# Optimization experiments

Hardware: AMD Instinct MI355X
Metric: run time of the kernel (lower is better)

The kernel has to match this reference:

```python
import jax, jax.numpy as jnp
import numpy as np

# Module hyperparameters (from init_kwargs)
KH = KW = 3
STRIDE = 2
PAD = 1
OUT_PAD = 1
DIL = 1
IN_LEN = 8   # length of each input capsule
OUT_LEN = 8  # length of each output capsule
N_IN_CAPS = 64 // IN_LEN    # 8
N_OUT_CAPS = 64 // OUT_LEN  # 8
NUM_ITERATIONS = 3


def _squash(x):
    # v * |v|^2 / ((1 + |v|^2) * |v|), along last (capsule-length) dim
    sn = jnp.sum(x * x, axis=-1, keepdims=True)
    return x * (sn / ((1.0 + sn) * jnp.sqrt(sn + 1e-12)))


def _k_means_routing(priors, num_iterations):
    # priors: [..., K, M] ; soft k-means routing with 'dot' similarity,
    # softmax over the votes dim K (softmax_dim=-2), squash at the end.
    out = jnp.mean(priors, axis=-2, keepdims=True)          # [..., 1, M]
    for _ in range(num_iterations):
        nrm = jnp.linalg.norm(out, axis=-1, keepdims=True)
        out_n = out / jnp.maximum(nrm, 1e-12)               # F.normalize(p=2)
        logits = jnp.sum(priors * out_n, axis=-1, keepdims=True)  # [..., K, 1]
        probs = jax.nn.softmax(logits, axis=-2)
        out = jnp.sum(probs * priors, axis=-2, keepdims=True)
    return _squash(out)[..., 0, :]                          # [..., M]


def setup_inputs() -> dict:
    key = jax.random.key(0)
    k1, k2, k3 = jax.random.split(key, 3)
    input = jax.random.normal(k1, (2, 64, 32, 32), dtype=jnp.float32)
    # weight: (in_length, out_channels//out_length, out_length, kh, kw)
    weight = jax.random.normal(k2, (IN_LEN, N_OUT_CAPS, OUT_LEN, KH, KW), dtype=jnp.float32) * 0.1
    # bias: (out_channels//out_length, out_length)
    bias = jax.random.normal(k3, (N_OUT_CAPS, OUT_LEN), dtype=jnp.float32) * 0.1
    return {"input": input, "weight": weight, "bias": bias}


def reference(input, weight, bias):
    n, c_in, h_in, w_in = input.shape
    fi = c_in // IN_LEN
    fo = weight.shape[1]
    # conv_transpose == conv(lhs-dilated input, spatially flipped kernel)
    pad_lo = DIL * (KH - 1) - PAD
    patches = jax.lax.conv_general_dilated_patches(
        input, (KH, KW), (1, 1),
        padding=((pad_lo, pad_lo + OUT_PAD), (pad_lo, pad_lo + OUT_PAD)),
        lhs_dilation=(STRIDE, STRIDE), rhs_dilation=(DIL, DIL))
    ho, wo = patches.shape[-2], patches.shape[-1]
    # feature dim of patches is ordered (c, kh, kw), channel-major
    patches = patches.reshape(n, fi, IN_LEN, KH, KW, ho, wo)
    w_flip = weight[..., ::-1, ::-1]  # [IN_LEN, fo, OUT_LEN, KH, KW]
    # votes: each (input capsule, kernel tap) casts a vote per output capsule
    priors = jnp.einsum('nflhwpq,lgmhw->npqgfhwm', patches, w_flip)
    priors = priors.reshape(n, ho, wo, fo, fi * KH * KW, OUT_LEN)
    out = _k_means_routing(priors, NUM_ITERATIONS)  # [n, ho, wo, fo, OUT_LEN]
    out = out + bias                                # bias: [fo, OUT_LEN]
    out = out.reshape(n, ho, wo, fo * OUT_LEN).transpose(0, 3, 1, 2)
    return out  # [n, out_channels, ho, wo] = [2, 64, 64, 64]
```

## Files before the change

kernel.cpp:

```cpp
#include <hip/hip_runtime.h>
#include <math.h>

#define HIN 32
#define WIN 32
#define NITER 3

__global__ __launch_bounds__(256) void transpose_in(const float* __restrict__ in,
                                                    float* __restrict__ tin) {
    __shared__ float lds[64 * 33];
    const int t = threadIdx.x;
    const int n = blockIdx.x >> 5;
    const int s0 = (blockIdx.x & 31) << 5;
    const float* ib = in + n * 65536;
    float* ob = tin + n * 65536;
#pragma unroll
    for (int k = 0; k < 8; ++k) {
        int idx = k * 256 + t;
        int c = idx >> 5, sl = idx & 31;
        lds[c * 33 + sl] = ib[c * 1024 + s0 + sl];
    }
    __syncthreads();
#pragma unroll
    for (int k = 0; k < 8; ++k) {
        int idx = k * 256 + t;
        int sl = idx >> 6, c = idx & 63;
        ob[(size_t)(s0 + sl) * 64 + c] = lds[c * 33 + sl];
    }
}

template <int CTRL>
__device__ __forceinline__ float dpp_add(float v) {
    int p = __builtin_amdgcn_update_dpp(0, __float_as_int(v), CTRL, 0xF, 0xF, true);
    return v + __int_as_float(p);
}
__device__ __forceinline__ float sum8(float v) {
    v = dpp_add<0xB1>(v);
    v = dpp_add<0x4E>(v);
    v = dpp_add<0x141>(v);
    return v;
}

template <int TH, int TW>
__device__ __forceinline__ void route_path(
    const float* __restrict__ tin, const float* __restrict__ wlds,
    const float* __restrict__ bias, float* __restrict__ olds,
    int n, int p, int q, int g, int s, int lane, int wave) {
    constexpr int T = TH * TW;
    constexpr float Z = (float)(72 - 8 * T);

    float pri[T][8];
#pragma unroll
    for (int i = 0; i < TH; ++i) {
        const int h = (TH == 1) ? 1 : i * 2;
        const int y = (p + h - 1) >> 1;
#pragma unroll
        for (int j = 0; j < TW; ++j) {
            const int w = (TW == 1) ? 1 : j * 2;
            const int x = (q + w - 1) >> 1;
            const int v = i * TW + j;
            const bool valid = (y < HIN) && (x < WIN);
            if (valid) {
                float xv[8];
                const float4* xp =
                    (const float4*)(tin + (((size_t)n * HIN + y) * WIN + x) * 64 + s * 8);
                float4 x0 = xp[0], x1 = xp[1];
                xv[0] = x0.x; xv[1] = x0.y; xv[2] = x0.z; xv[3] = x0.w;
                xv[4] = x1.x; xv[5] = x1.y; xv[6] = x1.z; xv[7] = x1.w;
                const int tap = h * 3 + w;
                const float* wb = wlds + (tap * 8 + g) * 64;
#pragma unroll
                for (int m = 0; m < 8; ++m) {
                    const float4* wp = (const float4*)(wb + ((m + g) & 7) * 8);
                    float4 w0 = wp[0], w1 = wp[1];
                    pri[v][m] = xv[0] * w0.x + xv[1] * w0.y + xv[2] * w0.z + xv[3] * w0.w +
                                xv[4] * w1.x + xv[5] * w1.y + xv[6] * w1.z + xv[7] * w1.w;
                }
            } else {
#pragma unroll
                for (int m = 0; m < 8; ++m) pri[v][m] = 0.f;
            }
        }
    }

    float o[8];
#pragma unroll
    for (int m = 0; m < 8; ++m) {
        float a = 0.f;
#pragma unroll
        for (int v = 0; v < T; ++v) a += pri[v][m];
        o[m] = sum8(a) * (1.f / 72.f);
    }

#pragma unroll
    for (int it = 0; it < NITER; ++it) {
        float sn = 0.f;
#pragma unroll
        for (int m = 0; m < 8; ++m) sn += o[m] * o[m];
        const float inv = __builtin_amdgcn_rsqf(fmaxf(sn, 1e-24f));
        float on[8];
#pragma unroll
        for (int m = 0; m < 8; ++m) on[m] = o[m] * inv;

        float r[9];
        r[8] = 0.f;
        float e[T];
#pragma unroll
        for (int v = 0; v < T; ++v) {
            float a = 0.f;
#pragma unroll
            for (int m = 0; m < 8; ++m) a += pri[v][m] * on[m];
            e[v] = __expf(a);
            r[8] += e[v];
        }
#pragma unroll
        for (int m = 0; m < 8; ++m) {
            float a = 0.f;
#pragma unroll
            for (int v = 0; v < T; ++v) a += e[v] * pri[v][m];
            r[m] = a;
        }
#pragma unroll
        for (int j = 0; j < 9; ++j) r[j] = sum8(r[j]);
        const float invs = __builtin_amdgcn_rcpf(r[8] + Z);
#pragma unroll
        for (int m = 0; m < 8; ++m) o[m] = r[m] * invs;
    }

    float sn = 0.f;
#pragma unroll
    for (int m = 0; m < 8; ++m) sn += o[m] * o[m];
    const float factor =
        sn * __builtin_amdgcn_rcpf(1.f + sn) * __builtin_amdgcn_rsqf(sn + 1e-12f);

    float val = o[0];
#pragma unroll
    for (int m = 1; m < 8; ++m)
        if (s == m) val = o[m];
    val = val * factor + bias[g * 8 + s];

    olds[lane * 5 + wave] = val;
}

__global__ __launch_bounds__(256) void caps_routing(
    const float* __restrict__ tin, const float* __restrict__ weight,
    const float* __restrict__ bias, float* __restrict__ out) {
    __shared__ float wlds[4608];
    __shared__ float olds[64 * 5];
    const int t = threadIdx.x;

    {
        const int l = t & 7;
        const int g8 = (t >> 3) & 7;
        const int c = t >> 6;
        const float* wsrc = weight + ((l * 8 + g8) * 8 + c * 2) * 9;
        float* wd = wlds + g8 * 64 + l;
#pragma unroll
        for (int mi = 0; mi < 2; ++mi) {
            const int mg = ((c * 2 + mi + g8) & 7) * 8;
#pragma unroll
            for (int kh = 0; kh < 3; ++kh)
#pragma unroll
                for (int kw = 0; kw < 3; ++kw) {
                    const int tap = (2 - kh) * 3 + (2 - kw);
                    wd[tap * 512 + mg] = wsrc[mi * 9 + kh * 3 + kw];
                }
        }
    }
    __syncthreads();

    const int wave = t >> 6;
    const int lane = t & 63;
    const int g = lane >> 3;
    const int s = lane & 7;

    const int b = blockIdx.x;
    const int n = b >> 10;
    const int p = (b >> 4) & 63;
    const int j = b & 15;
    const int qpar = j >> 3;
    const int qb = (j & 7) * 8 + qpar;
    const int q = qb + 2 * wave;

    if (p & 1) {
        if (qpar)
            route_path<2, 2>(tin, wlds, bias, olds, n, p, q, g, s, lane, wave);
        else
            route_path<2, 1>(tin, wlds, bias, olds, n, p, q, g, s, lane, wave);
    } else {
        if (qpar)
            route_path<1, 2>(tin, wlds, bias, olds, n, p, q, g, s, lane, wave);
        else
            route_path<1, 1>(tin, wlds, bias, olds, n, p, q, g, s, lane, wave);
    }

    __syncthreads();
    const int c2 = t >> 2, w = t & 3;
    out[(((size_t)n * 64 + c2) * 64 + p) * 64 + qb + 2 * w] = olds[c2 * 5 + w];
}

extern "C" void kernel_launch(void* const* d_in, const int* in_sizes, int n_in,
                              void* d_out, int out_size, void* d_ws, size_t ws_size,
                              hipStream_t stream) {
    const float* in = (const float*)d_in[0];
    const float* weight = (const float*)d_in[1];
    const float* bias = (const float*)d_in[2];
    float* out = (float*)d_out;
    float* tin = (float*)d_ws;

    transpose_in<<<64, 256, 0, stream>>>(in, tin);
    caps_routing<<<2048, 256, 0, stream>>>(tin, weight, bias, out);
}
```

Baseline: 75.49 us.

## Pre-permute weights in prep kernel and load only needed taps per block

Weight flipping and permutation move out of every routing block into one extra block of the prep kernel, which writes a pre-laid-out weight buffer to workspace. Each routing block then copies only the T taps its parity class needs (up to 4 of 9) into a smaller LDS array with contiguous float4 copies, replacing the strided scalar scatter of all 9 taps. The routing loop is also reorganized so the normalization by the softmax sum is applied only once at the end, because the direction-only normalize makes the per-iteration scale redundant. This cuts per-block prologue global loads, LDS writes and LDS footprint, at the cost of an extra workspace buffer and a dependency on the prep kernel.

```diff
diff --git a/kernel.cpp b/kernel.cpp
--- a/kernel.cpp
+++ b/kernel.cpp
@@ -4,27 +4,48 @@
 #define HIN 32
 #define WIN 32
 #define NITER 3
-
-__global__ __launch_bounds__(256) void transpose_in(const float* __restrict__ in,
-                                                    float* __restrict__ tin) {
+#define TIN_ELEMS 131072
+
+__global__ __launch_bounds__(256) void prep(const float* __restrict__ in,
+                                            const float* __restrict__ weight,
+                                            float* __restrict__ tin,
+                                            float* __restrict__ wprep) {
     __shared__ float lds[64 * 33];
+    const int b = blockIdx.x;
     const int t = threadIdx.x;
-    const int n = blockIdx.x >> 5;
-    const int s0 = (blockIdx.x & 31) << 5;
-    const float* ib = in + n * 65536;
-    float* ob = tin + n * 65536;
-#pragma unroll
-    for (int k = 0; k < 8; ++k) {
-        int idx = k * 256 + t;
-        int c = idx >> 5, sl = idx & 31;
-        lds[c * 33 + sl] = ib[c * 1024 + s0 + sl];
-    }
-    __syncthreads();
-#pragma unroll
-    for (int k = 0; k < 8; ++k) {
-        int idx = k * 256 + t;
-        int sl = idx >> 6, c = idx & 63;
-        ob[(size_t)(s0 + sl) * 64 + c] = lds[c * 33 + sl];
+    if (b < 64) {
+        const int n = b >> 5;
+        const int s0 = (b & 31) << 5;
+        const float* ib = in + n * 65536;
+        float* ob = tin + n * 65536;
+#pragma unroll
+        for (int k = 0; k < 8; ++k) {
+            int idx = k * 256 + t;
+            int c = idx >> 5, sl = idx & 31;
+            lds[c * 33 + sl] = ib[c * 1024 + s0 + sl];
+        }
+        __syncthreads();
+#pragma unroll
+        for (int k = 0; k < 8; ++k) {
+            int idx = k * 256 + t;
+            int sl = idx >> 6, c = idx & 63;
+            ob[(size_t)(s0 + sl) * 64 + c] = lds[c * 33 + sl];
+        }
+    } else {
+#pragma unroll
+        for (int k = 0; k < 2; ++k) {
+            const int lgm = k * 256 + t;
+            const int l = lgm >> 6, g = (lgm >> 3) & 7, m = lgm & 7;
+            const float* src = weight + lgm * 9;
+            float* drow = wprep + g * 64 + ((m + g) & 7) * 8 + l;
+#pragma unroll
+            for (int kh = 0; kh < 3; ++kh)
+#pragma unroll
+                for (int kw = 0; kw < 3; ++kw) {
+                    const int tap = (2 - kh) * 3 + (2 - kw);
+                    drow[tap * 512] = src[kh * 3 + kw];
+                }
+        }
     }
 }
 
@@ -41,12 +62,31 @@
 }
 
 template <int TH, int TW>
-__device__ __forceinline__ void route_path(
-    const float* __restrict__ tin, const float* __restrict__ wlds,
-    const float* __restrict__ bias, float* __restrict__ olds,
-    int n, int p, int q, int g, int s, int lane, int wave) {
+__device__ __forceinline__ void run_path(
+    const float* __restrict__ tin, const float* __restrict__ wprep,
+    const float* __restrict__ bias, float* __restrict__ out,
+    float* __restrict__ wlds, float* __restrict__ olds,
+    int t, int n, int p, int qb) {
     constexpr int T = TH * TW;
     constexpr float Z = (float)(72 - 8 * T);
+
+    const int wave = t >> 6;
+    const int lane = t & 63;
+
+    if (wave < T) {
+        const int hh = (TH == 1) ? 1 : ((TW == 2 ? (wave >> 1) : wave) * 2);
+        const int ww = (TW == 1) ? 1 : ((wave & 1) * 2);
+        const float4* src = (const float4*)(wprep + (hh * 3 + ww) * 512 + lane * 8);
+        float4 a = src[0], b2 = src[1];
+        float4* dst = (float4*)(wlds + wave * 512 + lane * 8);
+        dst[0] = a;
+        dst[1] = b2;
+    }
+    __syncthreads();
+
+    const int g = lane >> 3;
+    const int s = lane & 7;
+    const int q = qb + 2 * wave;
 
     float pri[T][8];
 #pragma unroll
@@ -55,9 +95,9 @@
         const int y = (p + h - 1) >> 1;
 #pragma unroll
         for (int j = 0; j < TW; ++j) {
+            const int v = i * TW + j;
             const int w = (TW == 1) ? 1 : j * 2;
             const int x = (q + w - 1) >> 1;
-            const int v = i * TW + j;
             const bool valid = (y < HIN) && (x < WIN);
             if (valid) {
                 float xv[8];
@@ -66,8 +106,7 @@
                 float4 x0 = xp[0], x1 = xp[1];
                 xv[0] = x0.x; xv[1] = x0.y; xv[2] = x0.z; xv[3] = x0.w;
                 xv[4] = x1.x; xv[5] = x1.y; xv[6] = x1.z; xv[7] = x1.w;
-                const int tap = h * 3 + w;
-                const float* wb = wlds + (tap * 8 + g) * 64;
+                const float* wb = wlds + (v * 8 + g) * 64;
 #pragma unroll
                 for (int m = 0; m < 8; ++m) {
                     const float4* wp = (const float4*)(wb + ((m + g) & 7) * 8);
@@ -82,27 +121,28 @@
         }
     }
 
-    float o[8];
+    float r[9];
 #pragma unroll
     for (int m = 0; m < 8; ++m) {
         float a = 0.f;
 #pragma unroll
         for (int v = 0; v < T; ++v) a += pri[v][m];
-        o[m] = sum8(a) * (1.f / 72.f);
-    }
+        r[m] = sum8(a);
+    }
+    r[8] = (float)T * 8.f;
 
 #pragma unroll
     for (int it = 0; it < NITER; ++it) {
         float sn = 0.f;
 #pragma unroll
-        for (int m = 0; m < 8; ++m) sn += o[m] * o[m];
+        for (int m = 0; m < 8; ++m) sn += r[m] * r[m];
         const float inv = __builtin_amdgcn_rsqf(fmaxf(sn, 1e-24f));
         float on[8];
 #pragma unroll
-        for (int m = 0; m < 8; ++m) on[m] = o[m] * inv;
-
-        float r[9];
-        r[8] = 0.f;
+        for (int m = 0; m < 8; ++m) on[m] = r[m] * inv;
+
+        float acc[9];
+        acc[8] = 0.f;
         float e[T];
 #pragma unroll
         for (int v = 0; v < T; ++v) {
@@ -110,21 +150,23 @@
 #pragma unroll
             for (int m = 0; m < 8; ++m) a += pri[v][m] * on[m];
             e[v] = __expf(a);
-            r[8] += e[v];
+            acc[8] += e[v];
         }
 #pragma unroll
         for (int m = 0; m < 8; ++m) {
             float a = 0.f;
 #pragma unroll
             for (int v = 0; v < T; ++v) a += e[v] * pri[v][m];
-            r[m] = a;
-        }
-#pragma unroll
-        for (int j = 0; j < 9; ++j) r[j] = sum8(r[j]);
-        const float invs = __builtin_amdgcn_rcpf(r[8] + Z);
-#pragma unroll
-        for (int m = 0; m < 8; ++m) o[m] = r[m] * invs;
-    }
+            acc[m] = a;
+        }
+#pragma unroll
+        for (int j = 0; j < 9; ++j) r[j] = sum8(acc[j]);
+    }
+
+    const float invs = __builtin_amdgcn_rcpf(r[8] + Z);
+    float o[8];
+#pragma unroll
+    for (int m = 0; m < 8; ++m) o[m] = r[m] * invs;
 
     float sn = 0.f;
 #pragma unroll
@@ -139,39 +181,18 @@
     val = val * factor + bias[g * 8 + s];
 
     olds[lane * 5 + wave] = val;
+
+    __syncthreads();
+    const int c2 = t >> 2, w = t & 3;
+    out[(((size_t)n * 64 + c2) * 64 + p) * 64 + qb + 2 * w] = olds[c2 * 5 + w];
 }
 
 __global__ __launch_bounds__(256) void caps_routing(
-    const float* __restrict__ tin, const float* __restrict__ weight,
+    const float* __restrict__ tin, const float* __restrict__ wprep,
     const float* __restrict__ bias, float* __restrict__ out) {
-    __shared__ float wlds[4608];
+    __shared__ float wlds[4 * 512];
     __shared__ float olds[64 * 5];
     const int t = threadIdx.x;
-
-    {
-        const int l = t & 7;
-        const int g8 = (t >> 3) & 7;
-        const int c = t >> 6;
-        const float* wsrc = weight + ((l * 8 + g8) * 8 + c * 2) * 9;
-        float* wd = wlds + g8 * 64 + l;
-#pragma unroll
-        for (int mi = 0; mi < 2; ++mi) {
-            const int mg = ((c * 2 + mi + g8) & 7) * 8;
-#pragma unroll
-            for (int kh = 0; kh < 3; ++kh)
-#pragma unroll
-                for (int kw = 0; kw < 3; ++kw) {
-                    const int tap = (2 - kh) * 3 + (2 - kw);
-                    wd[tap * 512 + mg] = wsrc[mi * 9 + kh * 3 + kw];
-                }
-        }
-    }
-    __syncthreads();
-
-    const int wave = t >> 6;
-    const int lane = t & 63;
-    const int g = lane >> 3;
-    const int s = lane & 7;
 
     const int b = blockIdx.x;
     const int n = b >> 10;
@@ -179,23 +200,18 @@
     const int j = b & 15;
     const int qpar = j >> 3;
     const int qb = (j & 7) * 8 + qpar;
-    const int q = qb + 2 * wave;
 
     if (p & 1) {
         if (qpar)
-            route_path<2, 2>(tin, wlds, bias, olds, n, p, q, g, s, lane, wave);
+            run_path<2, 2>(tin, wprep, bias, out, wlds, olds, t, n, p, qb);
         else
-            route_path<2, 1>(tin, wlds, bias, olds, n, p, q, g, s, lane, wave);
+            run_path<2, 1>(tin, wprep, bias, out, wlds, olds, t, n, p, qb);
     } else {
         if (qpar)
-            route_path<1, 2>(tin, wlds, bias, olds, n, p, q, g, s, lane, wave);
+            run_path<1, 2>(tin, wprep, bias, out, wlds, olds, t, n, p, qb);
         else
-            route_path<1, 1>(tin, wlds, bias, olds, n, p, q, g, s, lane, wave);
-    }
-
-    __syncthreads();
-    const int c2 = t >> 2, w = t & 3;
-    out[(((size_t)n * 64 + c2) * 64 + p) * 64 + qb + 2 * w] = olds[c2 * 5 + w];
+            run_path<1, 1>(tin, wprep, bias, out, wlds, olds, t, n, p, qb);
+    }
 }
 
 extern "C" void kernel_launch(void* const* d_in, const int* in_sizes, int n_in,
@@ -206,7 +222,8 @@
     const float* bias = (const float*)d_in[2];
     float* out = (float*)d_out;
     float* tin = (float*)d_ws;
-
-    transpose_in<<<64, 256, 0, stream>>>(in, tin);
-    caps_routing<<<2048, 256, 0, stream>>>(tin, weight, bias, out);
-}
+    float* wprep = (float*)d_ws + TIN_ELEMS;
+
+    prep<<<65, 256, 0, stream>>>(in, weight, tin, wprep);
+    caps_routing<<<2048, 256, 0, stream>>>(tin, wprep, bias, out);
+}
```

After: 74.56 us. About the same (-1.2%).
